# Kernel optimization log

Measured on AMD Instinct MI355X. Metric: run time of the kernel, lower is better.

Reference implementation:

```python
import jax, jax.numpy as jnp
import numpy as np

N_SAMPLES = 32768          # exp.n_samples = 2**15
TABLE_SIZE = 4096          # table_size init arg
STD = 0.01                 # hard-coded std fill in forward
WIN_EPS = 1e-8             # Window epsilon added to std
NORM_EPS = 1e-8            # max_norm epsilon (repo convention)


def setup_inputs() -> dict:
    key = jax.random.key(0)
    k1, k2 = jax.random.split(key)
    x = jax.random.normal(k1, (1, 1, N_SAMPLES), dtype=jnp.float32)        # unused by forward
    f0 = jax.random.uniform(k2, (1, 1), dtype=jnp.float32)                 # nn.Parameter uniform(0,1)
    table = jnp.sin(jnp.linspace(-np.pi, np.pi, TABLE_SIZE, dtype=jnp.float32))[None, :]  # (1, T)
    return {"x": x, "f0": f0, "table": table, "n_samples": N_SAMPLES}


def reference(x, f0, table, n_samples):
    table_size = table.shape[1]
    sigma = STD + WIN_EPS
    # phase accumulator: cumsum of constant |f0|, wrapped to [0, 1)
    f0a = jnp.abs(f0)                                                       # (1, 1)
    pos = jnp.mod(jnp.cumsum(jnp.broadcast_to(f0a, (1, n_samples)), axis=-1), 1.0)  # (1, N)
    mu = pos[:, :, None]                                                    # (1, N, 1); mn=0, scale=1
    rng = jnp.linspace(0.0, 1.0, table_size, dtype=x.dtype)[None, None, :]  # (1, 1, T)
    # Normal(mu, sigma).log_prob(rng), exponentiated -> Gaussian pdf windows
    log_norm = jnp.float32(-np.log(sigma) - 0.5 * np.log(2.0 * np.pi))
    z = (rng - mu) / sigma                                                  # (1, N, T) large intermediate
    windows = jnp.exp(-0.5 * z * z + log_norm)
    # max_norm: per-row normalize by max abs
    windows = windows / (jnp.max(jnp.abs(windows), axis=-1, keepdims=True) + NORM_EPS)
    # windows @ table.T : soft wavetable lookup reduction
    sig = jnp.einsum('bnt,ot->bno', windows, table)                         # (1, N, 1)
    return sig.reshape(1, 1, n_samples)
```

## Files before the change

kernel.cpp:

```cpp
#include <hip/hip_runtime.h>


#define NS     32768
#define TS     4096
#define BLK    256
#define LPS    8
#define SPB    (BLK / LPS)
#define NBLK   (NS / SPB)
#define HALF   144
#define NCHUNK 72
#define NTAP   (NCHUNK * 4)
#define TPAD   4352

__global__ __launch_bounds__(BLK) void wt_kernel(const float* __restrict__ f0p,
                                                 const float* __restrict__ table,
                                                 float* __restrict__ out)
{
    __shared__ __align__(16) float tab[TPAD];
    __shared__ __align__(16) float gtab[NTAP];
    const int tid = threadIdx.x;

    constexpr double SIGMA = 0.01 + 1e-8;
    constexpr double DZ    = 1.0 / (4095.0 * SIGMA);
    constexpr float  GC    = (float)(-0.5 * DZ * DZ);
    const float log_norm = 3.6862306527839187f;

    {
        const float4* t4 = (const float4*)table;
        float4* s4 = (float4*)tab;
        #pragma unroll
        for (int i = tid; i < TS / 4; i += BLK) s4[i] = t4[i];
        for (int i = TS / 4 + tid; i < TPAD / 4; i += BLK)
            s4[i] = make_float4(0.f, 0.f, 0.f, 0.f);
        for (int k = tid; k < NTAP; k += BLK) {
            const float kf = (float)k;
            gtab[k] = __expf(GC * kf * kf);
        }
    }
    const float f0a = fabsf(f0p[0]);
    __syncthreads();

    const int g = blockIdx.x * BLK + tid;
    const int n = g >> 3;
    const int j = g & (LPS - 1);

    const double mu = fmod((double)(n + 1) * (double)f0a, 1.0);

    const int tc = (int)(mu * 4095.0 + 0.5);
    const float zsf = (float)(((double)tc * (1.0 / 4095.0) - mu) / SIGMA);
    const float peak = __expf(fmaf(-0.5f * zsf, zsf, log_norm));
    const float denom = peak + 1e-8f;

    int t0 = tc - HALF;
    t0 = (t0 < 0) ? 0 : t0;
    t0 &= ~3;

    const double z0d = ((double)t0 * (1.0 / 4095.0) - mu) / SIGMA;
    const float  z0  = (float)z0d;
    const float  bb  = (float)(-z0d * DZ);

    const float e0  = __expf(fmaf(-0.5f * z0, z0, log_norm));
    const float r1  = __expf(bb);
    const float r32 = __expf(bb * 32.0f);
    float       rk  = __expf(bb * (float)(4 * j));
    const float r2  = r1 * r1;
    const float r3  = r2 * r1;

    const float4* __restrict__ src = (const float4*)(tab + t0);
    const float4* __restrict__ gsrc = (const float4*)gtab;
    float acc = 0.f;
    #pragma unroll
    for (int c = j; c < NCHUNK; c += LPS) {
        const float4 v  = src[c];
        const float4 gg = gsrc[c];
        const float w1 = rk * r1, w2 = rk * r2, w3 = rk * r3;
        acc = fmaf(rk * gg.x, v.x, acc);
        acc = fmaf(w1 * gg.y, v.y, acc);
        acc = fmaf(w2 * gg.z, v.z, acc);
        acc = fmaf(w3 * gg.w, v.w, acc);
        rk *= r32;
    }

    acc += __shfl_xor(acc, 1);
    acc += __shfl_xor(acc, 2);
    acc += __shfl_xor(acc, 4);
    if (j == 0) out[n] = acc * e0 / denom;
}

extern "C" void kernel_launch(void* const* d_in, const int* in_sizes, int n_in,
                              void* d_out, int out_size, void* d_ws, size_t ws_size,
                              hipStream_t stream)
{
    const float* f0    = (const float*)d_in[1];
    const float* table = (const float*)d_in[2];
    float* out = (float*)d_out;
    wt_kernel<<<dim3(NBLK), dim3(BLK), 0, stream>>>(f0, table, out);
}
```

Measured before the change: 9.595 us.

## Replace Gaussian tap table with recurrence, async LDS load, shrink window

```diff
diff --git a/kernel.cpp b/kernel.cpp
--- a/kernel.cpp
+++ b/kernel.cpp
@@ -7,35 +7,42 @@
 #define LPS    8
 #define SPB    (BLK / LPS)
 #define NBLK   (NS / SPB)
-#define HALF   144
-#define NCHUNK 72
-#define NTAP   (NCHUNK * 4)
-#define TPAD   4352
+#define HALF   128
+#define NCHUNK 64
+#define TPAD   4224
 
 __global__ __launch_bounds__(BLK) void wt_kernel(const float* __restrict__ f0p,
                                                  const float* __restrict__ table,
                                                  float* __restrict__ out)
 {
     __shared__ __align__(16) float tab[TPAD];
-    __shared__ __align__(16) float gtab[NTAP];
-    const int tid = threadIdx.x;
+    const int tid  = threadIdx.x;
+    const int wave = tid >> 6;
+    const int lane = tid & 63;
 
-    constexpr double SIGMA = 0.01 + 1e-8;
-    constexpr double DZ    = 1.0 / (4095.0 * SIGMA);
-    constexpr float  GC    = (float)(-0.5 * DZ * DZ);
+    constexpr double SIGMA   = 0.01 + 1e-8;
+    constexpr double INV_SG  = 1.0 / SIGMA;
+    constexpr double DZ      = 1.0 / (4095.0 * SIGMA);
+    constexpr double DZ2     = DZ * DZ;
     const float log_norm = 3.6862306527839187f;
+    const float C1 = (float)exp(-0.5 * DZ2 * 1.0);
+    const float C2 = (float)exp(-0.5 * DZ2 * 4.0);
+    const float C3 = (float)exp(-0.5 * DZ2 * 9.0);
+    const float T32 = (float)exp(-32.0 * DZ2);
+    const float MD  = (float)exp(-1024.0 * DZ2);
 
     {
         const float4* t4 = (const float4*)table;
-        float4* s4 = (float4*)tab;
         #pragma unroll
-        for (int i = tid; i < TS / 4; i += BLK) s4[i] = t4[i];
-        for (int i = TS / 4 + tid; i < TPAD / 4; i += BLK)
-            s4[i] = make_float4(0.f, 0.f, 0.f, 0.f);
-        for (int k = tid; k < NTAP; k += BLK) {
-            const float kf = (float)k;
-            gtab[k] = __expf(GC * kf * kf);
+        for (int it = 0; it < 4; ++it) {
+            const int f = it * 256 + wave * 64;
+            __builtin_amdgcn_global_load_lds(
+                (const __attribute__((address_space(1))) void*)(t4 + f + lane),
+                (__attribute__((address_space(3))) void*)(tab + 4 * f),
+                16, 0, 0);
         }
+        if (tid < (TPAD - TS) / 4)
+            ((float4*)tab)[TS / 4 + tid] = make_float4(0.f, 0.f, 0.f, 0.f);
     }
     const float f0a = fabsf(f0p[0]);
     __syncthreads();
@@ -47,7 +54,7 @@
     const double mu = fmod((double)(n + 1) * (double)f0a, 1.0);
 
     const int tc = (int)(mu * 4095.0 + 0.5);
-    const float zsf = (float)(((double)tc * (1.0 / 4095.0) - mu) / SIGMA);
+    const float zsf = (float)(((double)tc * (1.0 / 4095.0) - mu) * INV_SG);
     const float peak = __expf(fmaf(-0.5f * zsf, zsf, log_norm));
     const float denom = peak + 1e-8f;
 
@@ -55,30 +62,36 @@
     t0 = (t0 < 0) ? 0 : t0;
     t0 &= ~3;
 
-    const double z0d = ((double)t0 * (1.0 / 4095.0) - mu) / SIGMA;
+    const double z0d = ((double)t0 * (1.0 / 4095.0) - mu) * INV_SG;
     const float  z0  = (float)z0d;
     const float  bb  = (float)(-z0d * DZ);
 
     const float e0  = __expf(fmaf(-0.5f * z0, z0, log_norm));
     const float r1  = __expf(bb);
-    const float r32 = __expf(bb * 32.0f);
-    float       rk  = __expf(bb * (float)(4 * j));
-    const float r2  = r1 * r1;
-    const float r3  = r2 * r1;
+    const float R32 = __expf(bb * 32.0f);
+    const float k0f = (float)(4 * j);
+    float rk = __expf(bb * k0f);
+    float tch = __expf((float)(-DZ2) * k0f);
+    float gch = __expf((float)(-0.5 * DZ2) * k0f * k0f);
+    float mch = __expf((float)(-32.0 * DZ2) * k0f + (float)(-512.0 * DZ2));
 
     const float4* __restrict__ src = (const float4*)(tab + t0);
-    const float4* __restrict__ gsrc = (const float4*)gtab;
     float acc = 0.f;
     #pragma unroll
     for (int c = j; c < NCHUNK; c += LPS) {
-        const float4 v  = src[c];
-        const float4 gg = gsrc[c];
-        const float w1 = rk * r1, w2 = rk * r2, w3 = rk * r3;
-        acc = fmaf(rk * gg.x, v.x, acc);
-        acc = fmaf(w1 * gg.y, v.y, acc);
-        acc = fmaf(w2 * gg.z, v.z, acc);
-        acc = fmaf(w3 * gg.w, v.w, acc);
-        rk *= r32;
+        const float4 v = src[c];
+        const float A  = rk * gch;
+        const float s  = r1 * tch;
+        const float s2 = s * s;
+        const float s3 = s2 * s;
+        acc = fmaf(A,            v.x, acc);
+        acc = fmaf(A * s  * C1,  v.y, acc);
+        acc = fmaf(A * s2 * C2,  v.z, acc);
+        acc = fmaf(A * s3 * C3,  v.w, acc);
+        rk  *= R32;
+        gch *= mch;
+        mch *= MD;
+        tch *= T32;
     }
 
     acc += __shfl_xor(acc, 1);
```

New measurement: 12.21 us. 1.27x slower.
